# Kernel tuning notes

Measured on AMD Instinct MI355X. Metric: run time of the kernel, lower is better.

Reference implementation:

```python
import jax, jax.numpy as jnp
import numpy as np

B, H, S, D = 2, 16, 2048, 64


def setup_inputs() -> dict:
    key = jax.random.key(0)
    kq, kk, kv = jax.random.split(key, 3)
    q = jax.random.normal(kq, (B, H, S, D), dtype=jnp.float32)
    k = jax.random.normal(kk, (B, H, S, D), dtype=jnp.float32)
    v = jax.random.normal(kv, (B, H, S, D), dtype=jnp.float32)
    # causal mask: 1.0 where attention is DISALLOWED (strictly upper triangle)
    mask = jnp.triu(jnp.ones((S, S), dtype=jnp.float32), k=1)[None, None, :, :]
    return {"k": k, "q": q, "v": v, "mask": mask}


def reference(k, q, v, mask):
    d_k = jnp.asarray(k.shape[-1], dtype=jnp.float32)
    # scores: [B, H, S, S]
    scores = jnp.einsum("bhqd,bhkd->bhqk", q, k) / jnp.sqrt(d_k)
    scores = scores + mask * (-1e9)
    weights = jax.nn.softmax(scores, axis=-1)
    # attention output: [B, H, S, D]
    return jnp.einsum("bhqk,bhkd->bhqd", weights, v)
```

## Files before the change

kernel.cpp:

```cpp
#include <hip/hip_runtime.h>
#include <hip/hip_bf16.h>

typedef unsigned short ushort_t;
typedef __attribute__((ext_vector_type(8))) short v8s;
typedef __attribute__((ext_vector_type(4))) float v4f;

#define SEQ   2048
#define DH    64
#define BK    32
#define KSTR  72
#define VSTR  40
#define NHEADS 32
#define GBYTES 19456

#if __has_builtin(__builtin_amdgcn_exp2f)
#define EXP2(x) __builtin_amdgcn_exp2f(x)
#else
#define EXP2(x) exp2f(x)
#endif

__device__ __forceinline__ unsigned pkbf(float lo, float hi) {
    __hip_bfloat162 h = __float22bfloat162_rn(make_float2(lo, hi));
    union { __hip_bfloat162 h; unsigned u; } c; c.h = h; return c.u;
}

__device__ __forceinline__ v8s load8_bf_scaled(const float* p, float sc) {
    float4 a = *(const float4*)p;
    float4 b = *(const float4*)(p + 4);
    union { v8s v; unsigned u[4]; } t;
    t.u[0] = pkbf(a.x * sc, a.y * sc);
    t.u[1] = pkbf(a.z * sc, a.w * sc);
    t.u[2] = pkbf(b.x * sc, b.y * sc);
    t.u[3] = pkbf(b.z * sc, b.w * sc);
    return t.v;
}

__device__ __forceinline__ void process_tile_T(
    int kb, int myq0, int quad, int l15,
    v8s qa0, v8s qa1,
    v8s ka00, v8s ka01, v8s ka10, v8s ka11,
    v8s vb0, v8s vb1, v8s vb2, v8s vb3,
    v4f& a0, v4f& a1, v4f& a2, v4f& a3, float& ls)
{
    const v4f z = {0.f, 0.f, 0.f, 0.f};
    __builtin_amdgcn_s_setprio(1);
    v4f s0 = __builtin_amdgcn_mfma_f32_16x16x32_bf16(ka00, qa0, z, 0, 0, 0);
    s0     = __builtin_amdgcn_mfma_f32_16x16x32_bf16(ka01, qa1, s0, 0, 0, 0);
    v4f s1 = __builtin_amdgcn_mfma_f32_16x16x32_bf16(ka10, qa0, z, 0, 0, 0);
    s1     = __builtin_amdgcn_mfma_f32_16x16x32_bf16(ka11, qa1, s1, 0, 0, 0);
    __builtin_amdgcn_s_setprio(0);

    float p0[4], p1[4];
    if (kb + BK <= myq0) {
        #pragma unroll
        for (int r = 0; r < 4; ++r) { p0[r] = EXP2(s0[r]); p1[r] = EXP2(s1[r]); }
    } else {
        const int qrow = myq0 + l15;
        #pragma unroll
        for (int r = 0; r < 4; ++r) {
            p0[r] = (kb + 4 * quad + r      <= qrow) ? EXP2(s0[r]) : 0.f;
            p1[r] = (kb + 16 + 4 * quad + r <= qrow) ? EXP2(s1[r]) : 0.f;
        }
    }
    #pragma unroll
    for (int r = 0; r < 4; ++r) ls += p0[r] + p1[r];

    union { v8s v; unsigned u[4]; } pa;
    pa.u[0] = pkbf(p0[0], p0[1]); pa.u[1] = pkbf(p0[2], p0[3]);
    pa.u[2] = pkbf(p1[0], p1[1]); pa.u[3] = pkbf(p1[2], p1[3]);
    __builtin_amdgcn_s_setprio(1);
    a0 = __builtin_amdgcn_mfma_f32_16x16x32_bf16(pa.v, vb0, a0, 0, 0, 0);
    a1 = __builtin_amdgcn_mfma_f32_16x16x32_bf16(pa.v, vb1, a1, 0, 0, 0);
    a2 = __builtin_amdgcn_mfma_f32_16x16x32_bf16(pa.v, vb2, a2, 0, 0, 0);
    a3 = __builtin_amdgcn_mfma_f32_16x16x32_bf16(pa.v, vb3, a3, 0, 0, 0);
    __builtin_amdgcn_s_setprio(0);
}

__global__ __launch_bounds__(512, 4)
void attn_causal_dual(const float* __restrict__ Kg,
                      const float* __restrict__ Qg,
                      const float* __restrict__ Vg,
                      float* __restrict__ Og) {
    __shared__ alignas(16) unsigned char smem[2][GBYTES];

    const int i    = blockIdx.x;
    const int head = i & 31;
    const int j    = i >> 5;
    const int qt   = (j < 16) ? (31 - j) : (j - 16);
    const int qb   = qt * 64;
    const int tid  = threadIdx.x;
    const int w    = tid >> 6;
    const int grp  = w >> 2;
    const int wg   = w & 3;
    const int lane = tid & 63;
    const int l15  = lane & 15;
    const int quad = lane >> 4;

    const int niter = qt + 1;
    const int ktlo  = grp ? niter : 0;

    const int myq0 = qb + wg * 16, qmax = myq0 + 15;
    const size_t hb = (size_t)head * SEQ * DH;

    const float QSC = 0.125f * 1.4426950408889634f;
    v8s qa0, qa1;
    {
        const float* qp = Qg + hb + (size_t)(myq0 + l15) * DH + quad * 8;
        qa0 = load8_bf_scaled(qp, QSC);  qa1 = load8_bf_scaled(qp + 32, QSC);
    }

    v4f a0 = {0.f,0.f,0.f,0.f}, a1 = a0, a2 = a0, a3 = a0;
    float ls = 0.f;

    const int stid    = tid & 255;
    const int sk_kpos = stid >> 3;
    const int sk_d    = (stid & 7) * 8;
    const int sv_d    = stid & 63;

    const float* kbase  = Kg + hb + (size_t)sk_kpos * DH + sk_d;
    const float* vbaseA = Vg + hb + (size_t)(4 * wg) * DH + sv_d;
    const float* vbaseB = Vg + hb + (size_t)(16 + 4 * wg) * DH + sv_d;

    ushort_t* KtB = (ushort_t*)(smem[grp]);
    ushort_t* VtB = (ushort_t*)(smem[grp] + 9216);
    ushort_t* kdst0 = KtB + sk_kpos * KSTR + sk_d;
    ushort_t* vdst0 = VtB + sv_d * VSTR + 8 * wg;
    const int KOFS = BK * KSTR;
    const int VOFS = DH * VSTR;

    {
        const size_t t0 = (size_t)ktlo * BK * DH;
        float4 k0 = *(const float4*)(kbase + t0);
        float4 k1 = *(const float4*)(kbase + t0 + 4);
        float va[4], vb[4];
        #pragma unroll
        for (int m = 0; m < 4; ++m) {
            va[m] = vbaseA[t0 + (size_t)m * DH];
            vb[m] = vbaseB[t0 + (size_t)m * DH];
        }
        union { v8s v; unsigned u[4]; } kc, vc;
        kc.u[0] = pkbf(k0.x, k0.y); kc.u[1] = pkbf(k0.z, k0.w);
        kc.u[2] = pkbf(k1.x, k1.y); kc.u[3] = pkbf(k1.z, k1.w);
        vc.u[0] = pkbf(va[0], va[1]); vc.u[1] = pkbf(va[2], va[3]);
        vc.u[2] = pkbf(vb[0], vb[1]); vc.u[3] = pkbf(vb[2], vb[3]);
        *(v8s*)kdst0 = kc.v;
        *(v8s*)vdst0 = vc.v;
    }
    __syncthreads();

    for (int it = 0; it < niter; ++it) {
        const int kt  = ktlo + it;
        const int cur = it & 1;
        const bool havenext = (it + 1 < niter);

        float4 nk0, nk1; float nva[4], nvb[4];
        if (havenext) {
            const size_t toff = (size_t)(kt + 1) * BK * DH;
            nk0 = *(const float4*)(kbase + toff);
            nk1 = *(const float4*)(kbase + toff + 4);
            #pragma unroll
            for (int m = 0; m < 4; ++m) {
                nva[m] = vbaseA[toff + (size_t)m * DH];
                nvb[m] = vbaseB[toff + (size_t)m * DH];
            }
        }

        const int kb = kt * BK;
        if (kb <= qmax) {
            const ushort_t* KB = KtB + (cur ? KOFS : 0);
            const ushort_t* VB = VtB + (cur ? VOFS : 0);
            union { v8s v; uint4 u; } ka00, ka01, ka10, ka11, vb0, vb1, vb2, vb3;
            ka00.u = *(const uint4*)&KB[(l15)      * KSTR      + quad * 8];
            ka01.u = *(const uint4*)&KB[(l15)      * KSTR + 32 + quad * 8];
            ka10.u = *(const uint4*)&KB[(16 + l15) * KSTR      + quad * 8];
            ka11.u = *(const uint4*)&KB[(16 + l15) * KSTR + 32 + quad * 8];
            vb0.u  = *(const uint4*)&VB[(l15)      * VSTR + quad * 8];
            vb1.u  = *(const uint4*)&VB[(16 + l15) * VSTR + quad * 8];
            vb2.u  = *(const uint4*)&VB[(32 + l15) * VSTR + quad * 8];
            vb3.u  = *(const uint4*)&VB[(48 + l15) * VSTR + quad * 8];

            process_tile_T(kb, myq0, quad, l15, qa0, qa1,
                           ka00.v, ka01.v, ka10.v, ka11.v,
                           vb0.v, vb1.v, vb2.v, vb3.v,
                           a0, a1, a2, a3, ls);
        }

        if (havenext) {
            union { v8s v; unsigned u[4]; } kc, vc;
            kc.u[0] = pkbf(nk0.x, nk0.y); kc.u[1] = pkbf(nk0.z, nk0.w);
            kc.u[2] = pkbf(nk1.x, nk1.y); kc.u[3] = pkbf(nk1.z, nk1.w);
            vc.u[0] = pkbf(nva[0], nva[1]); vc.u[1] = pkbf(nva[2], nva[3]);
            vc.u[2] = pkbf(nvb[0], nvb[1]); vc.u[3] = pkbf(nvb[2], nvb[3]);
            const int nxt = cur ^ 1;
            *(v8s*)(kdst0 + (nxt ? KOFS : 0)) = kc.v;
            *(v8s*)(vdst0 + (nxt ? VOFS : 0)) = vc.v;
        }

        __syncthreads();
    }

    ls += __shfl_xor(ls, 16); ls += __shfl_xor(ls, 32);

    float* Ps = (float*)smem[0];
    float* Lp = (float*)smem[1];
    if (grp == 1) {
        #pragma unroll
        for (int r = 0; r < 4; ++r) {
            const int row = wg * 16 + 4 * quad + r;
            float* pr = Ps + row * 68 + l15;
            pr[0] = a0[r]; pr[16] = a1[r]; pr[32] = a2[r]; pr[48] = a3[r];
        }
        if (lane < 16) Lp[wg * 16 + l15] = ls;
    }
    __syncthreads();
    if (grp == 0) {
        const float lst = ls + Lp[wg * 16 + l15];
        #pragma unroll
        for (int r = 0; r < 4; ++r) {
            const float inv = 1.0f / __shfl(lst, 4 * quad + r);
            const int row = wg * 16 + 4 * quad + r;
            const float* pr = Ps + row * 68 + l15;
            float* op = Og + hb + (size_t)(qb + row) * DH + l15;
            op[0]  = (a0[r] + pr[0])  * inv;
            op[16] = (a1[r] + pr[16]) * inv;
            op[32] = (a2[r] + pr[32]) * inv;
            op[48] = (a3[r] + pr[48]) * inv;
        }
    }
}

extern "C" void kernel_launch(void* const* d_in, const int* in_sizes, int n_in,
                              void* d_out, int out_size, void* d_ws, size_t ws_size,
                              hipStream_t stream) {
    const float* K = (const float*)d_in[0];
    const float* Q = (const float*)d_in[1];
    const float* V = (const float*)d_in[2];
    float* O = (float*)d_out;
    attn_causal_dual<<<dim3(1024), 512, 0, stream>>>(K, Q, V, O);
}
```

Measured before the change: 142.1 us.

## Pre-convert K/V to bf16 tiled images in a prep kernel before attention

Adds a prep kernel that converts K to bf16 and V to bf16 in a pre-transposed, tile-ordered layout stored in the workspace. The attention kernel then loads one 16-byte uint4 per thread per tile instead of fp32 loads plus packing, which halves global traffic for K/V in the main loop and drops the conversion work. In exchange it adds a second kernel launch and a full fp32 read plus bf16 write pass over K and V. It falls back to the original kernel when the workspace is too small.

```diff
diff --git a/kernel.cpp b/kernel.cpp
--- a/kernel.cpp
+++ b/kernel.cpp
@@ -12,6 +12,7 @@
 #define VSTR  40
 #define NHEADS 32
 #define GBYTES 19456
+#define HELEMS 131072
 
 #if __has_builtin(__builtin_amdgcn_exp2f)
 #define EXP2(x) __builtin_amdgcn_exp2f(x)
@@ -76,11 +77,43 @@
     __builtin_amdgcn_s_setprio(0);
 }
 
+__global__ __launch_bounds__(256, 8)
+void attn_prep(const float* __restrict__ K, const float* __restrict__ V,
+               ushort_t* __restrict__ Kb, ushort_t* __restrict__ Vb) {
+    const int u = blockIdx.x * 256 + threadIdx.x;
+    if (u < 524288) {
+        const float* src = K + (size_t)u * 8;
+        float4 a = *(const float4*)src;
+        float4 b = *(const float4*)(src + 4);
+        union { v8s v; unsigned w[4]; } t;
+        t.w[0] = pkbf(a.x, a.y); t.w[1] = pkbf(a.z, a.w);
+        t.w[2] = pkbf(b.x, b.y); t.w[3] = pkbf(b.z, b.w);
+        *(v8s*)(Kb + (size_t)u * 8) = t.v;
+    } else {
+        const int q    = u - 524288;
+        const int d    = q & 63;
+        const int sgrp = (q >> 6) & 3;
+        const int tile = (q >> 8) & 63;
+        const int head = q >> 14;
+        const float* vsrc = V + ((size_t)head * SEQ + tile * 32) * DH + d;
+        float x[8];
+        #pragma unroll
+        for (int m = 0; m < 8; ++m) {
+            const int kpos = (m < 4) ? (4 * sgrp + m) : (16 + 4 * sgrp + (m - 4));
+            x[m] = vsrc[(size_t)kpos * DH];
+        }
+        union { v8s v; unsigned w[4]; } t;
+        t.w[0] = pkbf(x[0], x[1]); t.w[1] = pkbf(x[2], x[3]);
+        t.w[2] = pkbf(x[4], x[5]); t.w[3] = pkbf(x[6], x[7]);
+        *(v8s*)(Vb + (size_t)q * 8) = t.v;
+    }
+}
+
 __global__ __launch_bounds__(512, 4)
-void attn_causal_dual(const float* __restrict__ Kg,
-                      const float* __restrict__ Qg,
-                      const float* __restrict__ Vg,
-                      float* __restrict__ Og) {
+void attn_causal_dual2(const ushort_t* __restrict__ Kb,
+                       const float* __restrict__ Qg,
+                       const ushort_t* __restrict__ Vb,
+                       float* __restrict__ Og) {
     __shared__ alignas(16) unsigned char smem[2][GBYTES];
 
     const int i    = blockIdx.x;
@@ -116,33 +149,22 @@
     const int sk_kpos = stid >> 3;
     const int sk_d    = (stid & 7) * 8;
     const int sv_d    = stid & 63;
-
-    const float* kbase  = Kg + hb + (size_t)sk_kpos * DH + sk_d;
-    const float* vbaseA = Vg + hb + (size_t)(4 * wg) * DH + sv_d;
-    const float* vbaseB = Vg + hb + (size_t)(16 + 4 * wg) * DH + sv_d;
+    const int sv_g    = stid >> 6;
+
+    const ushort_t* ksrc = Kb + (size_t)head * HELEMS + stid * 8;
+    const ushort_t* vsrc = Vb + (size_t)head * HELEMS + stid * 8;
 
     ushort_t* KtB = (ushort_t*)(smem[grp]);
     ushort_t* VtB = (ushort_t*)(smem[grp] + 9216);
     ushort_t* kdst0 = KtB + sk_kpos * KSTR + sk_d;
-    ushort_t* vdst0 = VtB + sv_d * VSTR + 8 * wg;
+    ushort_t* vdst0 = VtB + sv_d * VSTR + sv_g * 8;
     const int KOFS = BK * KSTR;
     const int VOFS = DH * VSTR;
 
     {
-        const size_t t0 = (size_t)ktlo * BK * DH;
-        float4 k0 = *(const float4*)(kbase + t0);
-        float4 k1 = *(const float4*)(kbase + t0 + 4);
-        float va[4], vb[4];
-        #pragma unroll
-        for (int m = 0; m < 4; ++m) {
-            va[m] = vbaseA[t0 + (size_t)m * DH];
-            vb[m] = vbaseB[t0 + (size_t)m * DH];
-        }
-        union { v8s v; unsigned u[4]; } kc, vc;
-        kc.u[0] = pkbf(k0.x, k0.y); kc.u[1] = pkbf(k0.z, k0.w);
-        kc.u[2] = pkbf(k1.x, k1.y); kc.u[3] = pkbf(k1.z, k1.w);
-        vc.u[0] = pkbf(va[0], va[1]); vc.u[1] = pkbf(va[2], va[3]);
-        vc.u[2] = pkbf(vb[0], vb[1]); vc.u[3] = pkbf(vb[2], vb[3]);
+        union { v8s v; uint4 u; } kc, vc;
+        kc.u = *(const uint4*)(ksrc + (size_t)ktlo * 2048);
+        vc.u = *(const uint4*)(vsrc + (size_t)ktlo * 2048);
         *(v8s*)kdst0 = kc.v;
         *(v8s*)vdst0 = vc.v;
     }
@@ -153,16 +175,10 @@
         const int cur = it & 1;
         const bool havenext = (it + 1 < niter);
 
-        float4 nk0, nk1; float nva[4], nvb[4];
+        uint4 nk, nv;
         if (havenext) {
-            const size_t toff = (size_t)(kt + 1) * BK * DH;
-            nk0 = *(const float4*)(kbase + toff);
-            nk1 = *(const float4*)(kbase + toff + 4);
-            #pragma unroll
-            for (int m = 0; m < 4; ++m) {
-                nva[m] = vbaseA[toff + (size_t)m * DH];
-                nvb[m] = vbaseB[toff + (size_t)m * DH];
-            }
+            nk = *(const uint4*)(ksrc + (size_t)(kt + 1) * 2048);
+            nv = *(const uint4*)(vsrc + (size_t)(kt + 1) * 2048);
         }
 
         const int kb = kt * BK;
@@ -186,11 +202,8 @@
         }
 
         if (havenext) {
-            union { v8s v; unsigned u[4]; } kc, vc;
-            kc.u[0] = pkbf(nk0.x, nk0.y); kc.u[1] = pkbf(nk0.z, nk0.w);
-            kc.u[2] = pkbf(nk1.x, nk1.y); kc.u[3] = pkbf(nk1.z, nk1.w);
-            vc.u[0] = pkbf(nva[0], nva[1]); vc.u[1] = pkbf(nva[2], nva[3]);
-            vc.u[2] = pkbf(nvb[0], nvb[1]); vc.u[3] = pkbf(nvb[2], nvb[3]);
+            union { v8s v; uint4 u; } kc, vc;
+            kc.u = nk; vc.u = nv;
             const int nxt = cur ^ 1;
             *(v8s*)(kdst0 + (nxt ? KOFS : 0)) = kc.v;
             *(v8s*)(vdst0 + (nxt ? VOFS : 0)) = vc.v;
@@ -229,6 +242,159 @@
     }
 }
 
+__global__ __launch_bounds__(512, 4)
+void attn_causal_dual(const float* __restrict__ Kg,
+                      const float* __restrict__ Qg,
+                      const float* __restrict__ Vg,
+                      float* __restrict__ Og) {
+    __shared__ alignas(16) unsigned char smem[2][GBYTES];
+
+    const int i    = blockIdx.x;
+    const int head = i & 31;
+    const int j    = i >> 5;
+    const int qt   = (j < 16) ? (31 - j) : (j - 16);
+    const int qb   = qt * 64;
+    const int tid  = threadIdx.x;
+    const int w    = tid >> 6;
+    const int grp  = w >> 2;
+    const int wg   = w & 3;
+    const int lane = tid & 63;
+    const int l15  = lane & 15;
+    const int quad = lane >> 4;
+
+    const int niter = qt + 1;
+    const int ktlo  = grp ? niter : 0;
+
+    const int myq0 = qb + wg * 16, qmax = myq0 + 15;
+    const size_t hb = (size_t)head * SEQ * DH;
+
+    const float QSC = 0.125f * 1.4426950408889634f;
+    v8s qa0, qa1;
+    {
+        const float* qp = Qg + hb + (size_t)(myq0 + l15) * DH + quad * 8;
+        qa0 = load8_bf_scaled(qp, QSC);  qa1 = load8_bf_scaled(qp + 32, QSC);
+    }
+
+    v4f a0 = {0.f,0.f,0.f,0.f}, a1 = a0, a2 = a0, a3 = a0;
+    float ls = 0.f;
+
+    const int stid    = tid & 255;
+    const int sk_kpos = stid >> 3;
+    const int sk_d    = (stid & 7) * 8;
+    const int sv_d    = stid & 63;
+
+    const float* kbase  = Kg + hb + (size_t)sk_kpos * DH + sk_d;
+    const float* vbaseA = Vg + hb + (size_t)(4 * wg) * DH + sv_d;
+    const float* vbaseB = Vg + hb + (size_t)(16 + 4 * wg) * DH + sv_d;
+
+    ushort_t* KtB = (ushort_t*)(smem[grp]);
+    ushort_t* VtB = (ushort_t*)(smem[grp] + 9216);
+    ushort_t* kdst0 = KtB + sk_kpos * KSTR + sk_d;
+    ushort_t* vdst0 = VtB + sv_d * VSTR + 8 * wg;
+    const int KOFS = BK * KSTR;
+    const int VOFS = DH * VSTR;
+
+    {
+        const size_t t0 = (size_t)ktlo * BK * DH;
+        float4 k0 = *(const float4*)(kbase + t0);
+        float4 k1 = *(const float4*)(kbase + t0 + 4);
+        float va[4], vb[4];
+        #pragma unroll
+        for (int m = 0; m < 4; ++m) {
+            va[m] = vbaseA[t0 + (size_t)m * DH];
+            vb[m] = vbaseB[t0 + (size_t)m * DH];
+        }
+        union { v8s v; unsigned u[4]; } kc, vc;
+        kc.u[0] = pkbf(k0.x, k0.y); kc.u[1] = pkbf(k0.z, k0.w);
+        kc.u[2] = pkbf(k1.x, k1.y); kc.u[3] = pkbf(k1.z, k1.w);
+        vc.u[0] = pkbf(va[0], va[1]); vc.u[1] = pkbf(va[2], va[3]);
+        vc.u[2] = pkbf(vb[0], vb[1]); vc.u[3] = pkbf(vb[2], vb[3]);
+        *(v8s*)kdst0 = kc.v;
+        *(v8s*)vdst0 = vc.v;
+    }
+    __syncthreads();
+
+    for (int it = 0; it < niter; ++it) {
+        const int kt  = ktlo + it;
+        const int cur = it & 1;
+        const bool havenext = (it + 1 < niter);
+
+        float4 nk0, nk1; float nva[4], nvb[4];
+        if (havenext) {
+            const size_t toff = (size_t)(kt + 1) * BK * DH;
+            nk0 = *(const float4*)(kbase + toff);
+            nk1 = *(const float4*)(kbase + toff + 4);
+            #pragma unroll
+            for (int m = 0; m < 4; ++m) {
+                nva[m] = vbaseA[toff + (size_t)m * DH];
+                nvb[m] = vbaseB[toff + (size_t)m * DH];
+            }
+        }
+
+        const int kb = kt * BK;
+        if (kb <= qmax) {
+            const ushort_t* KB = KtB + (cur ? KOFS : 0);
+            const ushort_t* VB = VtB + (cur ? VOFS : 0);
+            union { v8s v; uint4 u; } ka00, ka01, ka10, ka11, vb0, vb1, vb2, vb3;
+            ka00.u = *(const uint4*)&KB[(l15)      * KSTR      + quad * 8];
+            ka01.u = *(const uint4*)&KB[(l15)      * KSTR + 32 + quad * 8];
+            ka10.u = *(const uint4*)&KB[(16 + l15) * KSTR      + quad * 8];
+            ka11.u = *(const uint4*)&KB[(16 + l15) * KSTR + 32 + quad * 8];
+            vb0.u  = *(const uint4*)&VB[(l15)      * VSTR + quad * 8];
+            vb1.u  = *(const uint4*)&VB[(16 + l15) * VSTR + quad * 8];
+            vb2.u  = *(const uint4*)&VB[(32 + l15) * VSTR + quad * 8];
+            vb3.u  = *(const uint4*)&VB[(48 + l15) * VSTR + quad * 8];
+
+            process_tile_T(kb, myq0, quad, l15, qa0, qa1,
+                           ka00.v, ka01.v, ka10.v, ka11.v,
+                           vb0.v, vb1.v, vb2.v, vb3.v,
+                           a0, a1, a2, a3, ls);
+        }
+
+        if (havenext) {
+            union { v8s v; unsigned u[4]; } kc, vc;
+            kc.u[0] = pkbf(nk0.x, nk0.y); kc.u[1] = pkbf(nk0.z, nk0.w);
+            kc.u[2] = pkbf(nk1.x, nk1.y); kc.u[3] = pkbf(nk1.z, nk1.w);
+            vc.u[0] = pkbf(nva[0], nva[1]); vc.u[1] = pkbf(nva[2], nva[3]);
+            vc.u[2] = pkbf(nvb[0], nvb[1]); vc.u[3] = pkbf(nvb[2], nvb[3]);
+            const int nxt = cur ^ 1;
+            *(v8s*)(kdst0 + (nxt ? KOFS : 0)) = kc.v;
+            *(v8s*)(vdst0 + (nxt ? VOFS : 0)) = vc.v;
+        }
+
+        __syncthreads();
+    }
+
+    ls += __shfl_xor(ls, 16); ls += __shfl_xor(ls, 32);
+
+    float* Ps = (float*)smem[0];
+    float* Lp = (float*)smem[1];
+    if (grp == 1) {
+        #pragma unroll
+        for (int r = 0; r < 4; ++r) {
+            const int row = wg * 16 + 4 * quad + r;
+            float* pr = Ps + row * 68 + l15;
+            pr[0] = a0[r]; pr[16] = a1[r]; pr[32] = a2[r]; pr[48] = a3[r];
+        }
+        if (lane < 16) Lp[wg * 16 + l15] = ls;
+    }
+    __syncthreads();
+    if (grp == 0) {
+        const float lst = ls + Lp[wg * 16 + l15];
+        #pragma unroll
+        for (int r = 0; r < 4; ++r) {
+            const float inv = 1.0f / __shfl(lst, 4 * quad + r);
+            const int row = wg * 16 + 4 * quad + r;
+            const float* pr = Ps + row * 68 + l15;
+            float* op = Og + hb + (size_t)(qb + row) * DH + l15;
+            op[0]  = (a0[r] + pr[0])  * inv;
+            op[16] = (a1[r] + pr[16]) * inv;
+            op[32] = (a2[r] + pr[32]) * inv;
+            op[48] = (a3[r] + pr[48]) * inv;
+        }
+    }
+}
+
 extern "C" void kernel_launch(void* const* d_in, const int* in_sizes, int n_in,
                               void* d_out, int out_size, void* d_ws, size_t ws_size,
                               hipStream_t stream) {
@@ -236,5 +402,16 @@
     const float* Q = (const float*)d_in[1];
     const float* V = (const float*)d_in[2];
     float* O = (float*)d_out;
-    attn_causal_dual<<<dim3(1024), 512, 0, stream>>>(K, Q, V, O);
-}
+
+    const size_t img_elems = (size_t)NHEADS * HELEMS;
+    const size_t need = 2 * img_elems * sizeof(ushort_t);
+
+    if (ws_size >= need) {
+        ushort_t* Kb = (ushort_t*)d_ws;
+        ushort_t* Vb = Kb + img_elems;
+        attn_prep<<<dim3(4096), 256, 0, stream>>>(K, V, Kb, Vb);
+        attn_causal_dual2<<<dim3(1024), 512, 0, stream>>>(Kb, Q, Vb, O);
+    } else {
+        attn_causal_dual<<<dim3(1024), 512, 0, stream>>>(K, Q, V, O);
+    }
+}
```

Result: no change. 140.4 us (-1.2%).

## Pre-convert K/V to bf16 fragment layout and run single-wave attention kernel

Applied to the files above, without the earlier changes.

Adds a prep kernel that converts K and V into bf16 tiles already arranged in MFMA fragment order in the workspace. A new one-wave-per-block attention kernel then reads those fragments straight into registers with prefetch, handling 32 query rows per wave, with no shared memory or barriers. This removes the LDS staging, per-iteration conversion and block syncs of the old kernel. In exchange it costs an extra kernel launch, an extra workspace round trip, and much lower per-block parallelism, and it falls back to the old kernel if the workspace is too small.

```diff
diff --git a/kernel.cpp b/kernel.cpp
--- a/kernel.cpp
+++ b/kernel.cpp
@@ -12,6 +12,7 @@
 #define VSTR  40
 #define NHEADS 32
 #define GBYTES 19456
+#define HELEMS 131072
 
 #if __has_builtin(__builtin_amdgcn_exp2f)
 #define EXP2(x) __builtin_amdgcn_exp2f(x)
@@ -76,6 +77,130 @@
     __builtin_amdgcn_s_setprio(0);
 }
 
+__global__ __launch_bounds__(256, 8)
+void attn_prep(const float* __restrict__ K, const float* __restrict__ V,
+               ushort_t* __restrict__ Kf, ushort_t* __restrict__ Vf) {
+    const int u = blockIdx.x * 256 + threadIdx.x;
+    if (u < 524288) {
+        const int lane = u & 63;
+        const int l15  = lane & 15, quad = lane >> 4;
+        const int f    = (u >> 6) & 3;
+        const int kt   = (u >> 8) & 63;
+        const int head = u >> 14;
+        const int row  = kt * 32 + ((f & 2) ? 16 : 0) + l15;
+        const int col  = ((f & 1) ? 32 : 0) + quad * 8;
+        const float* src = K + ((size_t)head * SEQ + row) * DH + col;
+        float4 a = *(const float4*)src;
+        float4 b = *(const float4*)(src + 4);
+        union { v8s v; unsigned w[4]; } t;
+        t.w[0] = pkbf(a.x, a.y); t.w[1] = pkbf(a.z, a.w);
+        t.w[2] = pkbf(b.x, b.y); t.w[3] = pkbf(b.z, b.w);
+        *(v8s*)(Kf + (size_t)u * 8) = t.v;
+    } else {
+        const int q    = u - 524288;
+        const int lane = q & 63;
+        const int l15  = lane & 15, qd = lane >> 4;
+        const int b    = (q >> 6) & 3;
+        const int kt   = (q >> 8) & 63;
+        const int head = q >> 14;
+        const float* vsrc = V + ((size_t)head * SEQ + kt * 32) * DH + (l15 + 16 * b);
+        float x[8];
+        #pragma unroll
+        for (int j = 0; j < 8; ++j) {
+            const int kpos = (j < 4) ? (4 * qd + j) : (16 + 4 * qd + (j - 4));
+            x[j] = vsrc[(size_t)kpos * DH];
+        }
+        union { v8s v; unsigned w[4]; } t;
+        t.w[0] = pkbf(x[0], x[1]); t.w[1] = pkbf(x[2], x[3]);
+        t.w[2] = pkbf(x[4], x[5]); t.w[3] = pkbf(x[6], x[7]);
+        *(v8s*)(Vf + (size_t)q * 8) = t.v;
+    }
+}
+
+__global__ __launch_bounds__(64, 2)
+void attn_causal_wave(const ushort_t* __restrict__ Kf,
+                      const float* __restrict__ Qg,
+                      const ushort_t* __restrict__ Vf,
+                      float* __restrict__ Og) {
+    const int i    = blockIdx.x;
+    const int head = i & 31;
+    const int c    = 63 - (i >> 5);
+    const int qb   = c * 32;
+    const int lane = threadIdx.x;
+    const int l15  = lane & 15;
+    const int quad = lane >> 4;
+    const int myqA = qb, myqB = qb + 16;
+    const size_t hb = (size_t)head * SEQ * DH;
+
+    const float QSC = 0.125f * 1.4426950408889634f;
+    v8s qaA0, qaA1, qaB0, qaB1;
+    {
+        const float* qpA = Qg + hb + (size_t)(myqA + l15) * DH + quad * 8;
+        const float* qpB = Qg + hb + (size_t)(myqB + l15) * DH + quad * 8;
+        qaA0 = load8_bf_scaled(qpA, QSC); qaA1 = load8_bf_scaled(qpA + 32, QSC);
+        qaB0 = load8_bf_scaled(qpB, QSC); qaB1 = load8_bf_scaled(qpB + 32, QSC);
+    }
+
+    v4f aA0 = {0.f,0.f,0.f,0.f}, aA1 = aA0, aA2 = aA0, aA3 = aA0;
+    v4f aB0 = aA0, aB1 = aA0, aB2 = aA0, aB3 = aA0;
+    float lsA = 0.f, lsB = 0.f;
+
+    const ushort_t* kf = Kf + (size_t)head * HELEMS + lane * 8;
+    const ushort_t* vf = Vf + (size_t)head * HELEMS + lane * 8;
+    const int nt = c + 1;
+
+    union U { v8s v; uint4 u; };
+    U k0c, k1c, k2c, k3c, v0c, v1c, v2c, v3c;
+    {
+        k0c.u = *(const uint4*)(kf);        k1c.u = *(const uint4*)(kf + 512);
+        k2c.u = *(const uint4*)(kf + 1024); k3c.u = *(const uint4*)(kf + 1536);
+        v0c.u = *(const uint4*)(vf);        v1c.u = *(const uint4*)(vf + 512);
+        v2c.u = *(const uint4*)(vf + 1024); v3c.u = *(const uint4*)(vf + 1536);
+    }
+
+    for (int kt = 0; kt < nt; ++kt) {
+        U k0n, k1n, k2n, k3n, v0n, v1n, v2n, v3n;
+        const bool havenext = (kt + 1 < nt);
+        if (havenext) {
+            const ushort_t* kp = kf + (size_t)(kt + 1) * 2048;
+            const ushort_t* vp = vf + (size_t)(kt + 1) * 2048;
+            k0n.u = *(const uint4*)(kp);        k1n.u = *(const uint4*)(kp + 512);
+            k2n.u = *(const uint4*)(kp + 1024); k3n.u = *(const uint4*)(kp + 1536);
+            v0n.u = *(const uint4*)(vp);        v1n.u = *(const uint4*)(vp + 512);
+            v2n.u = *(const uint4*)(vp + 1024); v3n.u = *(const uint4*)(vp + 1536);
+        }
+
+        const int kb = kt * BK;
+        process_tile_T(kb, myqA, quad, l15, qaA0, qaA1,
+                       k0c.v, k1c.v, k2c.v, k3c.v,
+                       v0c.v, v1c.v, v2c.v, v3c.v,
+                       aA0, aA1, aA2, aA3, lsA);
+        process_tile_T(kb, myqB, quad, l15, qaB0, qaB1,
+                       k0c.v, k1c.v, k2c.v, k3c.v,
+                       v0c.v, v1c.v, v2c.v, v3c.v,
+                       aB0, aB1, aB2, aB3, lsB);
+
+        if (havenext) {
+            k0c = k0n; k1c = k1n; k2c = k2n; k3c = k3n;
+            v0c = v0n; v1c = v1n; v2c = v2n; v3c = v3n;
+        }
+    }
+
+    lsA += __shfl_xor(lsA, 16); lsA += __shfl_xor(lsA, 32);
+    lsB += __shfl_xor(lsB, 16); lsB += __shfl_xor(lsB, 32);
+    #pragma unroll
+    for (int r = 0; r < 4; ++r) {
+        const float invA = 1.0f / __shfl(lsA, 4 * quad + r);
+        const float invB = 1.0f / __shfl(lsB, 4 * quad + r);
+        float* opA = Og + hb + (size_t)(myqA + 4 * quad + r) * DH + l15;
+        float* opB = Og + hb + (size_t)(myqB + 4 * quad + r) * DH + l15;
+        opA[0]  = aA0[r] * invA; opA[16] = aA1[r] * invA;
+        opA[32] = aA2[r] * invA; opA[48] = aA3[r] * invA;
+        opB[0]  = aB0[r] * invB; opB[16] = aB1[r] * invB;
+        opB[32] = aB2[r] * invB; opB[48] = aB3[r] * invB;
+    }
+}
+
 __global__ __launch_bounds__(512, 4)
 void attn_causal_dual(const float* __restrict__ Kg,
                       const float* __restrict__ Qg,
@@ -201,25 +326,25 @@
 
     ls += __shfl_xor(ls, 16); ls += __shfl_xor(ls, 32);
 
-    float* Ps = (float*)smem[0];
-    float* Lp = (float*)smem[1];
+    float* Ps2 = (float*)smem[0];
+    float* Lp2 = (float*)smem[1];
     if (grp == 1) {
         #pragma unroll
         for (int r = 0; r < 4; ++r) {
             const int row = wg * 16 + 4 * quad + r;
-            float* pr = Ps + row * 68 + l15;
+            float* pr = Ps2 + row * 68 + l15;
             pr[0] = a0[r]; pr[16] = a1[r]; pr[32] = a2[r]; pr[48] = a3[r];
         }
-        if (lane < 16) Lp[wg * 16 + l15] = ls;
+        if (lane < 16) Lp2[wg * 16 + l15] = ls;
     }
     __syncthreads();
     if (grp == 0) {
-        const float lst = ls + Lp[wg * 16 + l15];
+        const float lst = ls + Lp2[wg * 16 + l15];
         #pragma unroll
         for (int r = 0; r < 4; ++r) {
             const float inv = 1.0f / __shfl(lst, 4 * quad + r);
             const int row = wg * 16 + 4 * quad + r;
-            const float* pr = Ps + row * 68 + l15;
+            const float* pr = Ps2 + row * 68 + l15;
             float* op = Og + hb + (size_t)(qb + row) * DH + l15;
             op[0]  = (a0[r] + pr[0])  * inv;
             op[16] = (a1[r] + pr[16]) * inv;
@@ -236,5 +361,16 @@
     const float* Q = (const float*)d_in[1];
     const float* V = (const float*)d_in[2];
     float* O = (float*)d_out;
-    attn_causal_dual<<<dim3(1024), 512, 0, stream>>>(K, Q, V, O);
-}
+
+    const size_t img_elems = (size_t)NHEADS * HELEMS;
+    const size_t need = 2 * img_elems * sizeof(ushort_t);
+
+    if (ws_size >= need) {
+        ushort_t* Kf = (ushort_t*)d_ws;
+        ushort_t* Vf = Kf + img_elems;
+        attn_prep<<<dim3(4096), 256, 0, stream>>>(K, V, Kf, Vf);
+        attn_causal_wave<<<dim3(2048), 64, 0, stream>>>(Kf, Q, Vf, O);
+    } else {
+        attn_causal_dual<<<dim3(1024), 512, 0, stream>>>(K, Q, V, O);
+    }
+}
```

Measured after the change: 141.4 us. About the same (-0.4%).
